# Performance work log

Measured on AMD Instinct MI355X. Metric: run time of the kernel, lower is better.

Reference implementation:

```python
import jax, jax.numpy as jnp
import numpy as np

N = 100000
E = 1600000
NFEAT = 256
NHID = 64
NHEADS = 4
NCLASS = 32
ALPHA = 0.2  # LeakyReLU negative slope


def _xavier_normal(key, shape, gain=1.414):
    fan_in, fan_out = shape[-2], shape[-1]
    std = gain * np.sqrt(2.0 / (fan_in + fan_out))
    return (jax.random.normal(key, shape, jnp.float32) * std).astype(jnp.float32)


def setup_inputs() -> dict:
    key = jax.random.key(0)
    k = jax.random.split(key, 8)
    x = jax.random.normal(k[0], (N, NFEAT), jnp.float32)
    src = jax.random.randint(k[1], (E,), 0, N, jnp.int32)
    dst = jax.random.randint(k[2], (E,), 0, N, jnp.int32)
    # self-loops on the first N edges so every row has nonzero attention mass
    loop = jnp.arange(N, dtype=jnp.int32)
    src = src.at[:N].set(loop)
    dst = dst.at[:N].set(loop)
    edge_index = jnp.stack([src, dst])  # [2, E]
    W_heads = _xavier_normal(k[3], (NHEADS, NFEAT, NHID))
    # torch inits a as (1, 2*out): xavier fans are (2*out, 1)
    a_std = 1.414 * np.sqrt(2.0 / (2 * NHID + 1))
    a_heads = (jax.random.normal(k[4], (NHEADS, 2 * NHID), jnp.float32) * a_std)
    W_out = _xavier_normal(k[5], (NHEADS * NHID, NCLASS))
    a_out_std = 1.414 * np.sqrt(2.0 / (2 * NCLASS + 1))
    a_out = (jax.random.normal(k[6], (2 * NCLASS,), jnp.float32) * a_out_std)
    return {"x": x, "edge_index": edge_index, "W_heads": W_heads,
            "a_heads": a_heads, "W_out": W_out, "a_out": a_out}


def _gat_layer(x, W, a, src, dst):
    """One sparse GAT attention layer (dropout = identity, eval mode)."""
    h = x @ W                      # [N, O]
    O = W.shape[1]
    s_src = h @ a[:O]              # [N]
    s_dst = h @ a[O:]              # [N]
    # e_ij = exp(-leakyrelu(a . [h_i ; h_j])) for edge (i=src, j=dst)
    e = jnp.exp(-jax.nn.leaky_relu(s_src[src] + s_dst[dst], ALPHA))  # [E]
    rowsum = jax.ops.segment_sum(e, src, num_segments=N)             # [N]
    agg = jax.ops.segment_sum(e[:, None] * h[dst], src, num_segments=N)  # [N, O]
    return agg / rowsum[:, None]


def reference(x, edge_index, W_heads, a_heads, W_out, a_out):
    src, dst = edge_index[0], edge_index[1]
    # multi-head hidden layer (concat=True -> elu per head)
    heads = jax.vmap(lambda W, a: _gat_layer(x, W, a, src, dst))(W_heads, a_heads)  # [H, N, NHID]
    x1 = jax.nn.elu(heads).transpose(1, 0, 2).reshape(N, NHEADS * NHID)
    # output attention layer (concat=False), then elu + log_softmax in SpGAT.forward
    h2 = _gat_layer(x1, W_out, a_out, src, dst)  # [N, NCLASS]
    return jax.nn.log_softmax(jax.nn.elu(h2), axis=1)
```

## Files before the change

### kernel.cpp

```cpp
#include <hip/hip_runtime.h>
#include <cstdint>
#include <cstddef>

#define ALPHA 0.2f

__device__ __forceinline__ float lrelu(float x) { return x > 0.f ? x : ALPHA * x; }

__device__ __forceinline__ float qbf(float x)
{
    uint32_t u = __float_as_uint(x);
    uint32_t r = (u + 0x7FFFu + ((u >> 16) & 1u)) & 0xFFFF0000u;
    return __uint_as_float(r);
}

__device__ __forceinline__ float readlane_f(float v, int l)
{
    return __int_as_float(__builtin_amdgcn_readlane(__float_as_int(v), l));
}

__global__ __launch_bounds__(256) void k_gemm1(const float* __restrict__ x,
                                               const float* __restrict__ Wh,
                                               const float* __restrict__ a,
                                               float* __restrict__ H,
                                               float* __restrict__ s1src,
                                               float* __restrict__ s1dst, int n)
{
    __shared__ float As[32][68];
    __shared__ float Bs[32][256];
    __shared__ float Pa[64][17];
    __shared__ float Pb[64][17];
    __shared__ float avs[256], avd[256];
    const int tid = threadIdx.x;
    const int row0 = blockIdx.x * 64;
    const int tx = tid & 15, ty = tid >> 4;

    {
        int h = tid >> 6, o = tid & 63;
        avs[tid] = qbf(a[h * 128 + o]);
        avd[tid] = qbf(a[h * 128 + 64 + o]);
    }

    float acc[4][16];
#pragma unroll
    for (int r = 0; r < 4; ++r)
#pragma unroll
        for (int c = 0; c < 16; ++c) acc[r][c] = 0.f;

    for (int k0 = 0; k0 < 256; k0 += 32) {
        for (int j = tid; j < 512; j += 256) {
            int r = j >> 3, kk = (j & 7) << 2;
            int gr = row0 + r; if (gr >= n) gr = n - 1;
            const float4 v = *(const float4*)&x[(size_t)gr * 256 + k0 + kk];
            As[kk + 0][r] = qbf(v.x); As[kk + 1][r] = qbf(v.y);
            As[kk + 2][r] = qbf(v.z); As[kk + 3][r] = qbf(v.w);
        }
        for (int j = tid; j < 2048; j += 256) {
            int kk = j >> 6, c4 = j & 63;
            int h = c4 >> 4, o = (c4 & 15) << 2;
            const float4 v = *(const float4*)&Wh[h * 16384 + (k0 + kk) * 64 + o];
            float* bp = &Bs[kk][c4 << 2];
            bp[0] = qbf(v.x); bp[1] = qbf(v.y); bp[2] = qbf(v.z); bp[3] = qbf(v.w);
        }
        __syncthreads();
#pragma unroll
        for (int kk = 0; kk < 32; ++kk) {
            const float4 av4 = *(const float4*)&As[kk][ty << 2];
            const float4 b0 = *(const float4*)&Bs[kk][tx * 16 + 0];
            const float4 b1 = *(const float4*)&Bs[kk][tx * 16 + 4];
            const float4 b2 = *(const float4*)&Bs[kk][tx * 16 + 8];
            const float4 b3 = *(const float4*)&Bs[kk][tx * 16 + 12];
            const float av[4]  = {av4.x, av4.y, av4.z, av4.w};
            const float bv[16] = {b0.x, b0.y, b0.z, b0.w, b1.x, b1.y, b1.z, b1.w,
                                  b2.x, b2.y, b2.z, b2.w, b3.x, b3.y, b3.z, b3.w};
#pragma unroll
            for (int r = 0; r < 4; ++r)
#pragma unroll
                for (int c = 0; c < 16; ++c) acc[r][c] += av[r] * bv[c];
        }
        __syncthreads();
    }
#pragma unroll
    for (int r = 0; r < 4; ++r) {
        int row = (ty << 2) + r;
        int gr = row0 + row;
        float ps = 0.f, pd = 0.f;
#pragma unroll
        for (int c = 0; c < 16; ++c) {
            ps += acc[r][c] * avs[tx * 16 + c];
            pd += acc[r][c] * avd[tx * 16 + c];
        }
        Pa[row][tx] = ps;
        Pb[row][tx] = pd;
        if (gr < n) {
            float* dst = &H[(size_t)gr * 256 + tx * 16];
#pragma unroll
            for (int i = 0; i < 4; ++i)
                *(float4*)&dst[4 * i] = make_float4(acc[r][4 * i + 0], acc[r][4 * i + 1],
                                                    acc[r][4 * i + 2], acc[r][4 * i + 3]);
        }
    }
    __syncthreads();
    for (int o = tid; o < 512; o += 256) {
        int row = o >> 3, h = (o >> 1) & 3, which = o & 1;
        const float* P = which ? &Pb[row][0] : &Pa[row][0];
        float s = P[h * 4 + 0] + P[h * 4 + 1] + P[h * 4 + 2] + P[h * 4 + 3];
        int gr = row0 + row;
        if (gr < n) {
            if (which) s1dst[gr * 4 + h] = s;
            else       s1src[gr * 4 + h] = s;
        }
    }
}

__global__ void k_zero(int* __restrict__ p, int n)
{
    int i = blockIdx.x * 256 + threadIdx.x;
    if (i < n) p[i] = 0;
}

__global__ void k_hist(const int* __restrict__ src, int* __restrict__ counts, int e)
{
    int i = blockIdx.x * 256 + threadIdx.x;
    if (i < e) atomicAdd(&counts[src[i]], 1);
}

__global__ __launch_bounds__(256) void k_blocksum(const int* __restrict__ counts,
                                                  int* __restrict__ bsum, int n)
{
    int tid = threadIdx.x;
    int i0 = blockIdx.x * 2048 + tid * 8;
    int s = 0;
#pragma unroll
    for (int k = 0; k < 8; ++k) {
        int i = i0 + k;
        if (i < n) s += counts[i];
    }
#pragma unroll
    for (int m = 32; m >= 1; m >>= 1) s += __shfl_xor(s, m);
    __shared__ int ws[4];
    int lane = tid & 63, wv = tid >> 6;
    if (lane == 0) ws[wv] = s;
    __syncthreads();
    if (tid == 0) bsum[blockIdx.x] = ws[0] + ws[1] + ws[2] + ws[3];
}

__global__ void k_scanmeta(const int* __restrict__ bsum, int* __restrict__ choff, int nchunk)
{
    int lane = threadIdx.x;
    int v = (lane < nchunk) ? bsum[lane] : 0;
    int incl = v;
#pragma unroll
    for (int d = 1; d < 64; d <<= 1) {
        int t = __shfl_up(incl, d);
        if (lane >= d) incl += t;
    }
    if (lane < nchunk) choff[lane] = incl - v;
}

__global__ __launch_bounds__(256) void k_apply(const int* __restrict__ counts,
                                               const int* __restrict__ choff,
                                               int* __restrict__ offsets,
                                               int* __restrict__ cursor, int n)
{
    int tid = threadIdx.x;
    int i0 = blockIdx.x * 2048 + tid * 8;
    int c[8]; int s = 0;
#pragma unroll
    for (int k = 0; k < 8; ++k) {
        int i = i0 + k;
        c[k] = (i < n) ? counts[i] : 0;
        s += c[k];
    }
    int lane = tid & 63, wv = tid >> 6;
    int incl = s;
#pragma unroll
    for (int d = 1; d < 64; d <<= 1) {
        int t = __shfl_up(incl, d);
        if (lane >= d) incl += t;
    }
    __shared__ int ws[4];
    if (lane == 63) ws[wv] = incl;
    __syncthreads();
    int woff = 0;
    for (int w = 0; w < 4; ++w)
        if (w < wv) woff += ws[w];
    int run = incl - s + woff + choff[blockIdx.x];
#pragma unroll
    for (int k = 0; k < 8; ++k) {
        int i = i0 + k;
        if (i < n) { offsets[i] = run; cursor[i] = run; }
        run += c[k];
        if (i == n - 1) offsets[n] = run;
    }
}

__global__ void k_scatter(const int* __restrict__ src,
                          int* __restrict__ cursor, int* __restrict__ csr, int e)
{
    int i = blockIdx.x * 256 + threadIdx.x;
    if (i < e) {
        int pos = atomicAdd(&cursor[src[i]], 1);
        csr[pos] = i;
    }
}

__global__ __launch_bounds__(256) void k_sortcsr(const int* __restrict__ offsets,
                                                 int* __restrict__ csr, int n)
{
    int gtid = blockIdx.x * 256 + threadIdx.x;
    int node = gtid >> 6, lane = gtid & 63;
    if (node >= n) return;
    int beg = offsets[node], end = offsets[node + 1];
    int cnt = end - beg;
    if (cnt <= 0) return;
    if (cnt <= 64) {
        int v = (lane < cnt) ? csr[beg + lane] : 0x7FFFFFFF;
#pragma unroll
        for (int k = 2; k <= 64; k <<= 1) {
#pragma unroll
            for (int j = k >> 1; j > 0; j >>= 1) {
                int o = __shfl_xor(v, j);
                bool up    = ((lane & k) == 0);
                bool lower = ((lane & j) == 0);
                int mn = min(v, o), mx = max(v, o);
                v = (lower == up) ? mn : mx;
            }
        }
        if (lane < cnt) csr[beg + lane] = v;
    } else {
        if (lane == 0) {
            for (int i = beg + 1; i < end; ++i) {
                int key = csr[i]; int j = i - 1;
                while (j >= beg && csr[j] > key) { csr[j + 1] = csr[j]; --j; }
                csr[j + 1] = key;
            }
        }
    }
}

__global__ void k_w1(const int* __restrict__ csr_eid,
                     const int* __restrict__ src, const int* __restrict__ dst,
                     const float* __restrict__ s1src, const float* __restrict__ s1dst,
                     int* __restrict__ csrd, float* __restrict__ w1, int e)
{
    int i = blockIdx.x * 256 + threadIdx.x;
    if (i >= e) return;
    int eid = csr_eid[i];
    int s = src[eid], d = dst[eid];
    csrd[i] = d;
    const float4 aa = *(const float4*)&s1src[(size_t)s * 4];
    const float4 bb = *(const float4*)&s1dst[(size_t)d * 4];
    float4 w;
    w.x = expf(-lrelu(aa.x + bb.x));
    w.y = expf(-lrelu(aa.y + bb.y));
    w.z = expf(-lrelu(aa.z + bb.z));
    w.w = expf(-lrelu(aa.w + bb.w));
    *(float4*)&w1[(size_t)i * 4] = w;
}

__global__ void k_w2(const int* __restrict__ csr_eid,
                     const int* __restrict__ src, const int* __restrict__ dst,
                     const float* __restrict__ s2src, const float* __restrict__ s2dst,
                     float* __restrict__ w2, int e)
{
    int i = blockIdx.x * 256 + threadIdx.x;
    if (i >= e) return;
    int eid = csr_eid[i];
    float z = s2src[src[eid]] + s2dst[dst[eid]];
    w2[i] = expf(-lrelu(z));
}

__global__ __launch_bounds__(256) void k_agg1(const int* __restrict__ csrd,
                                              const int* __restrict__ offsets,
                                              const float* __restrict__ H,
                                              const float* __restrict__ w1,
                                              const float* __restrict__ Wout,
                                              const float* __restrict__ aout,
                                              float* __restrict__ h2,
                                              float* __restrict__ s2src,
                                              float* __restrict__ s2dst, int n)
{
    __shared__ float Wt[32][256];
    const int tid = threadIdx.x;
    for (int j = tid; j < 8192; j += 256) {
        int c = j >> 8, k = j & 255;
        Wt[c][k] = qbf(Wout[k * 32 + c]);
    }
    __syncthreads();

    int gtid = blockIdx.x * 256 + tid;
    int node = gtid >> 6, lane = gtid & 63;
    if (node >= n) return;
    const int beg = offsets[node], end = offsets[node + 1];
    const int wsel = lane & 48;
    float ax = 0.f, ay = 0.f, az = 0.f, aw = 0.f, wsum = 0.f;
    for (int j = beg; j < end; j += 16) {
        int slot = j + (lane & 15);
        bool okl = slot < end;
        int dv   = okl ? csrd[slot] : 0;
        float wv = okl ? w1[(size_t)slot * 4 + (lane >> 4)] : 0.f;
        int cnt = min(16, end - j);
        int d = __builtin_amdgcn_readlane(dv, 0);
        float4 hv = *(const float4*)&H[(size_t)d * 256 + lane * 4];
        int t = 0;
        for (; t + 1 < cnt; ++t) {
            int d2 = __builtin_amdgcn_readlane(dv, t + 1);
            float4 hv2 = *(const float4*)&H[(size_t)d2 * 256 + lane * 4];
            float w = __shfl(wv, wsel + t);
            ax += w * hv.x; ay += w * hv.y; az += w * hv.z; aw += w * hv.w;
            wsum += w;
            hv = hv2;
        }
        float w = __shfl(wv, wsel + t);
        ax += w * hv.x; ay += w * hv.y; az += w * hv.z; aw += w * hv.w;
        wsum += w;
    }
    float inv = 1.f / wsum;
    float r0 = ax * inv, r1 = ay * inv, r2 = az * inv, r3 = aw * inv;
    r0 = r0 > 0.f ? r0 : expm1f(r0);
    r1 = r1 > 0.f ? r1 : expm1f(r1);
    r2 = r2 > 0.f ? r2 : expm1f(r2);
    r3 = r3 > 0.f ? r3 : expm1f(r3);

    float p[32];
#pragma unroll
    for (int c = 0; c < 32; ++c) {
        const float4 wv4 = *(const float4*)&Wt[c][lane << 2];
        p[c] = r0 * wv4.x + r1 * wv4.y + r2 * wv4.z + r3 * wv4.w;
    }
#pragma unroll
    for (int m = 32; m >= 1; m >>= 1) {
#pragma unroll
        for (int c = 0; c < 32; ++c) p[c] += __shfl_xor(p[c], m);
    }
    if (lane == 0) {
        float ss = 0.f, sd2 = 0.f;
#pragma unroll
        for (int c = 0; c < 32; ++c) {
            ss  += p[c] * qbf(aout[c]);
            sd2 += p[c] * qbf(aout[32 + c]);
        }
        float* dst = &h2[(size_t)node * 32];
#pragma unroll
        for (int i = 0; i < 8; ++i)
            *(float4*)&dst[4 * i] = make_float4(p[4 * i + 0], p[4 * i + 1],
                                                p[4 * i + 2], p[4 * i + 3]);
        s2src[node] = ss;
        s2dst[node] = sd2;
    }
}

__global__ __launch_bounds__(256) void k_agg2(const int* __restrict__ csrd,
                                              const int* __restrict__ offsets,
                                              const float* __restrict__ h2,
                                              const float* __restrict__ w2,
                                              float* __restrict__ out, int n)
{
    int gtid = blockIdx.x * 256 + threadIdx.x;
    int node = gtid >> 6, lane = gtid & 63;
    if (node >= n) return;
    int c = lane & 31;
    int beg = offsets[node], end = offsets[node + 1];
    float acc = 0.f, wsum = 0.f;
    for (int j = beg; j < end; j += 64) {
        int slot = j + lane;
        bool okl = slot < end;
        int dv    = okl ? csrd[slot] : 0;
        float wvv = okl ? w2[slot] : 0.f;
        int cnt = min(64, end - j);
        int d = __builtin_amdgcn_readlane(dv, 0);
        float hv = h2[(size_t)d * 32 + c];
        int t = 0;
        for (; t + 1 < cnt; ++t) {
            int d2 = __builtin_amdgcn_readlane(dv, t + 1);
            float hv2 = h2[(size_t)d2 * 32 + c];
            float w = readlane_f(wvv, t);
            acc += w * hv; wsum += w;
            hv = hv2;
        }
        float w = readlane_f(wvv, t);
        acc += w * hv; wsum += w;
    }
    float v = acc / wsum;
    v = v > 0.f ? v : expm1f(v);
    float m = v;
#pragma unroll
    for (int i = 16; i >= 1; i >>= 1) m = fmaxf(m, __shfl_xor(m, i));
    float ex = expf(v - m);
    float se = ex;
#pragma unroll
    for (int i = 16; i >= 1; i >>= 1) se += __shfl_xor(se, i);
    float r = v - m - logf(se);
    if (lane < 32) out[(size_t)node * 32 + c] = r;
}

extern "C" void kernel_launch(void* const* d_in, const int* in_sizes, int n_in,
                              void* d_out, int out_size, void* d_ws, size_t ws_size,
                              hipStream_t stream)
{
    const float* x    = (const float*)d_in[0];
    const int*   ei   = (const int*)d_in[1];
    const float* Wh   = (const float*)d_in[2];
    const float* ah   = (const float*)d_in[3];
    const float* Wout = (const float*)d_in[4];
    const float* aout = (const float*)d_in[5];
    float* out = (float*)d_out;

    const int n = in_sizes[0] / 256;
    const int e = in_sizes[1] / 2;
    const int* src = ei;
    const int* dst = ei + e;

    auto align = [](size_t v) { return (v + 255) & ~(size_t)255; };
    char* w = (char*)d_ws;
    float* H      = (float*)w; w += align((size_t)n * 256 * 4);
    float* h2     = (float*)w; w += align((size_t)n * 32 * 4);
    int*   csr    = (int*)w;   w += align((size_t)e * 4);
    int*   csrd   = (int*)w;   w += align((size_t)e * 4);
    float* w1     = (float*)w; w += align((size_t)e * 4 * 4);
    float* w2     = (float*)w; w += align((size_t)e * 4);
    float* s1src  = (float*)w; w += align((size_t)n * 4 * 4);
    float* s1dst  = (float*)w; w += align((size_t)n * 4 * 4);
    int*   counts = (int*)w;   w += align((size_t)n * 4);
    int*   offs   = (int*)w;   w += align((size_t)(n + 1) * 4);
    int*   cursor = (int*)w;   w += align((size_t)n * 4);
    float* s2src  = (float*)w; w += align((size_t)n * 4);
    float* s2dst  = (float*)w; w += align((size_t)n * 4);
    int*   bsum   = (int*)w;   w += align(4096);
    int*   choff  = (int*)w;   w += align(4096);

    const int nchunk = (n + 2047) / 2048;
    const int gN256  = (n + 255) / 256;
    const int gWave  = (n + 3) / 4;
    const int gE     = (e + 255) / 256;

    k_gemm1<<<(n + 63) / 64, 256, 0, stream>>>(x, Wh, ah, H, s1src, s1dst, n);

    k_zero<<<gN256, 256, 0, stream>>>(counts, n);
    k_hist<<<gE, 256, 0, stream>>>(src, counts, e);
    k_blocksum<<<nchunk, 256, 0, stream>>>(counts, bsum, n);
    k_scanmeta<<<1, 64, 0, stream>>>(bsum, choff, nchunk);
    k_apply<<<nchunk, 256, 0, stream>>>(counts, choff, offs, cursor, n);
    k_scatter<<<gE, 256, 0, stream>>>(src, cursor, csr, e);
    k_sortcsr<<<gWave, 256, 0, stream>>>(offs, csr, n);

    k_w1<<<gE, 256, 0, stream>>>(csr, src, dst, s1src, s1dst, csrd, w1, e);

    k_agg1<<<gWave, 256, 0, stream>>>(csrd, offs, H, w1, Wout, aout,
                                      h2, s2src, s2dst, n);
    k_w2<<<gE, 256, 0, stream>>>(csr, src, dst, s2src, s2dst, w2, e);

    k_agg2<<<gWave, 256, 0, stream>>>(csrd, offs, h2, w2, out, n);
}
```

Baseline: 1.311 ms.

## Store hidden features as bf16 and deepen gather prefetch in aggregation kernels

The first-layer GEMM now writes H as packed bf16 instead of fp32, which halves the bytes gathered per edge in the first aggregation. That aggregation loop is restructured to keep four neighbor rows in flight, padding the tail to a multiple of four. The second aggregation splits edges between the two half-waves, so each lane handles alternate edges, and combines the halves with a cross-lane reduction. Storing H in bf16 adds rounding error. Existing qbf rounding of weights suggests reduced precision is tolerated, but the output accuracy margin could shrink.

```diff
diff --git a/kernel.cpp b/kernel.cpp
--- a/kernel.cpp
+++ b/kernel.cpp
@@ -13,15 +13,24 @@
     return __uint_as_float(r);
 }
 
-__device__ __forceinline__ float readlane_f(float v, int l)
-{
-    return __int_as_float(__builtin_amdgcn_readlane(__float_as_int(v), l));
+__device__ __forceinline__ uint32_t bfbits(float x)
+{
+    uint32_t u = __float_as_uint(x);
+    return (u + 0x7FFFu + ((u >> 16) & 1u)) >> 16;
+}
+__device__ __forceinline__ uint32_t pack2(float lo, float hi)
+{
+    return bfbits(lo) | (bfbits(hi) << 16);
+}
+__device__ __forceinline__ float bf2f(ushort u)
+{
+    return __uint_as_float(((uint32_t)u) << 16);
 }
 
 __global__ __launch_bounds__(256) void k_gemm1(const float* __restrict__ x,
                                                const float* __restrict__ Wh,
                                                const float* __restrict__ a,
-                                               float* __restrict__ H,
+                                               ushort* __restrict__ Hb,
                                                float* __restrict__ s1src,
                                                float* __restrict__ s1dst, int n)
 {
@@ -92,11 +101,14 @@
         Pa[row][tx] = ps;
         Pb[row][tx] = pd;
         if (gr < n) {
-            float* dst = &H[(size_t)gr * 256 + tx * 16];
-#pragma unroll
-            for (int i = 0; i < 4; ++i)
-                *(float4*)&dst[4 * i] = make_float4(acc[r][4 * i + 0], acc[r][4 * i + 1],
-                                                    acc[r][4 * i + 2], acc[r][4 * i + 3]);
+            uint32_t* dst = (uint32_t*)&Hb[(size_t)gr * 256 + tx * 16];
+            uint4 u0, u1;
+            u0.x = pack2(acc[r][0],  acc[r][1]);  u0.y = pack2(acc[r][2],  acc[r][3]);
+            u0.z = pack2(acc[r][4],  acc[r][5]);  u0.w = pack2(acc[r][6],  acc[r][7]);
+            u1.x = pack2(acc[r][8],  acc[r][9]);  u1.y = pack2(acc[r][10], acc[r][11]);
+            u1.z = pack2(acc[r][12], acc[r][13]); u1.w = pack2(acc[r][14], acc[r][15]);
+            *(uint4*)&dst[0] = u0;
+            *(uint4*)&dst[4] = u1;
         }
     }
     __syncthreads();
@@ -272,7 +284,7 @@
 
 __global__ __launch_bounds__(256) void k_agg1(const int* __restrict__ csrd,
                                               const int* __restrict__ offsets,
-                                              const float* __restrict__ H,
+                                              const ushort* __restrict__ Hb,
                                               const float* __restrict__ w1,
                                               const float* __restrict__ Wout,
                                               const float* __restrict__ aout,
@@ -293,28 +305,37 @@
     if (node >= n) return;
     const int beg = offsets[node], end = offsets[node + 1];
     const int wsel = lane & 48;
+    const int lo4 = lane * 4;
     float ax = 0.f, ay = 0.f, az = 0.f, aw = 0.f, wsum = 0.f;
+
+#define LDH(T) (*(const ushort4*)&Hb[(size_t)__builtin_amdgcn_readlane(dv, (T)) * 256 + lo4])
+#define CONS(B, T) { float w_ = __shfl(wv, wsel + (T));                         \
+        ax += w_ * bf2f((B).x); ay += w_ * bf2f((B).y);                         \
+        az += w_ * bf2f((B).z); aw += w_ * bf2f((B).w); wsum += w_; }
+
     for (int j = beg; j < end; j += 16) {
         int slot = j + (lane & 15);
         bool okl = slot < end;
         int dv   = okl ? csrd[slot] : 0;
         float wv = okl ? w1[(size_t)slot * 4 + (lane >> 4)] : 0.f;
-        int cnt = min(16, end - j);
-        int d = __builtin_amdgcn_readlane(dv, 0);
-        float4 hv = *(const float4*)&H[(size_t)d * 256 + lane * 4];
-        int t = 0;
-        for (; t + 1 < cnt; ++t) {
-            int d2 = __builtin_amdgcn_readlane(dv, t + 1);
-            float4 hv2 = *(const float4*)&H[(size_t)d2 * 256 + lane * 4];
-            float w = __shfl(wv, wsel + t);
-            ax += w * hv.x; ay += w * hv.y; az += w * hv.z; aw += w * hv.w;
-            wsum += w;
-            hv = hv2;
-        }
-        float w = __shfl(wv, wsel + t);
-        ax += w * hv.x; ay += w * hv.y; az += w * hv.z; aw += w * hv.w;
-        wsum += w;
-    }
+        int cnt  = min(16, end - j);
+        int cntr = (cnt + 3) & ~3;
+        ushort4 b0 = LDH(0), b1 = LDH(1), b2 = LDH(2), b3 = LDH(3);
+        for (int t0 = 0; t0 < cntr; t0 += 4) {
+            ushort4 c0 = b0, c1 = b1, c2 = b2, c3 = b3;
+            if (t0 + 4 < cntr) {
+                int t4 = t0 + 4;
+                c0 = LDH(t4 + 0); c1 = LDH(t4 + 1);
+                c2 = LDH(t4 + 2); c3 = LDH(t4 + 3);
+            }
+            CONS(b0, t0 + 0); CONS(b1, t0 + 1);
+            CONS(b2, t0 + 2); CONS(b3, t0 + 3);
+            b0 = c0; b1 = c1; b2 = c2; b3 = c3;
+        }
+    }
+#undef LDH
+#undef CONS
+
     float inv = 1.f / wsum;
     float r0 = ax * inv, r1 = ay * inv, r2 = az * inv, r3 = aw * inv;
     r0 = r0 > 0.f ? r0 : expm1f(r0);
@@ -359,28 +380,33 @@
     int gtid = blockIdx.x * 256 + threadIdx.x;
     int node = gtid >> 6, lane = gtid & 63;
     if (node >= n) return;
-    int c = lane & 31;
+    int c = lane & 31, p = lane >> 5;
     int beg = offsets[node], end = offsets[node + 1];
     float acc = 0.f, wsum = 0.f;
+
     for (int j = beg; j < end; j += 64) {
         int slot = j + lane;
         bool okl = slot < end;
         int dv    = okl ? csrd[slot] : 0;
         float wvv = okl ? w2[slot] : 0.f;
-        int cnt = min(64, end - j);
-        int d = __builtin_amdgcn_readlane(dv, 0);
-        float hv = h2[(size_t)d * 32 + c];
-        int t = 0;
-        for (; t + 1 < cnt; ++t) {
-            int d2 = __builtin_amdgcn_readlane(dv, t + 1);
-            float hv2 = h2[(size_t)d2 * 32 + c];
-            float w = readlane_f(wvv, t);
-            acc += w * hv; wsum += w;
-            hv = hv2;
-        }
-        float w = readlane_f(wvv, t);
-        acc += w * hv; wsum += w;
-    }
+        int cnt  = min(64, end - j);
+        int cntr = (cnt + 1) & ~1;
+        int t = p;
+        int d0 = __shfl(dv, t);
+        float h0 = h2[(size_t)d0 * 32 + c];
+        for (; t + 2 < cntr; t += 2) {
+            int d1 = __shfl(dv, t + 2);
+            float h1 = h2[(size_t)d1 * 32 + c];
+            float w = __shfl(wvv, t);
+            acc += w * h0; wsum += w;
+            h0 = h1;
+        }
+        float w = __shfl(wvv, t);
+        acc += w * h0; wsum += w;
+    }
+
+    acc += __shfl_xor(acc, 32);
+    wsum += __shfl_xor(wsum, 32);
     float v = acc / wsum;
     v = v > 0.f ? v : expm1f(v);
     float m = v;
@@ -413,7 +439,7 @@
 
     auto align = [](size_t v) { return (v + 255) & ~(size_t)255; };
     char* w = (char*)d_ws;
-    float* H      = (float*)w; w += align((size_t)n * 256 * 4);
+    ushort* Hb    = (ushort*)w; w += align((size_t)n * 256 * 2);
     float* h2     = (float*)w; w += align((size_t)n * 32 * 4);
     int*   csr    = (int*)w;   w += align((size_t)e * 4);
     int*   csrd   = (int*)w;   w += align((size_t)e * 4);
@@ -434,7 +460,7 @@
     const int gWave  = (n + 3) / 4;
     const int gE     = (e + 255) / 256;
 
-    k_gemm1<<<(n + 63) / 64, 256, 0, stream>>>(x, Wh, ah, H, s1src, s1dst, n);
+    k_gemm1<<<(n + 63) / 64, 256, 0, stream>>>(x, Wh, ah, Hb, s1src, s1dst, n);
 
     k_zero<<<gN256, 256, 0, stream>>>(counts, n);
     k_hist<<<gE, 256, 0, stream>>>(src, counts, e);
@@ -446,7 +472,7 @@
 
     k_w1<<<gE, 256, 0, stream>>>(csr, src, dst, s1src, s1dst, csrd, w1, e);
 
-    k_agg1<<<gWave, 256, 0, stream>>>(csrd, offs, H, w1, Wout, aout,
+    k_agg1<<<gWave, 256, 0, stream>>>(csrd, offs, Hb, w1, Wout, aout,
                                       h2, s2src, s2dst, n);
     k_w2<<<gE, 256, 0, stream>>>(csr, src, dst, s2src, s2dst, w2, e);
 
```

Result: no change. 1.325 ms (+1.1%).
